# Kernel tuning notes

Hardware: AMD Instinct MI355X
Metric: run time of the kernel (lower is better)

Reference implementation:

```python
import jax, jax.numpy as jnp
import numpy as np
from jax import lax

B, C, H, W = 8, 64, 50, 65
K = 3
N = H * W            # 3250 attention positions
NR = N - 1           # 3249 = 57^2 rotary positions (first token unrotated)
SIDE = float(np.sqrt(NR))  # 57.0, exact
THETA = 10.0
EPS = 1e-5


def setup_inputs() -> dict:
    key = jax.random.key(0)
    ks = jax.random.split(key, 6)
    x = jax.random.normal(ks[0], (B, C, H, W), jnp.float32)
    s = 1.0 / np.sqrt(C * K * K)
    wq = jax.random.normal(ks[1], (C, C, K, K), jnp.float32) * s
    wk = jax.random.normal(ks[2], (C, C, K, K), jnp.float32) * s
    wv = jax.random.normal(ks[3], (C, C, K, K), jnp.float32) * s
    bq = jnp.zeros((C,), jnp.float32)
    bk = jnp.zeros((C,), jnp.float32)
    bv = jnp.zeros((C,), jnp.float32)
    # init_2d_freqs with num_heads=1, rotate=True, viewed as (2, C//2)
    mag = 1.0 / THETA ** (jnp.arange(0, C, 4, dtype=jnp.float32)[: C // 4] / C)
    ang = float(jax.random.uniform(ks[4])) * 2.0 * np.pi
    fx = jnp.concatenate([mag * np.cos(ang), mag * np.cos(np.pi / 2 + ang)])
    fy = jnp.concatenate([mag * np.sin(ang), mag * np.sin(np.pi / 2 + ang)])
    freqs = jnp.stack([fx, fy], axis=0)  # (2, C//2)
    gamma = jnp.zeros((1,), jnp.float32)
    bn_weight = jnp.ones((C,), jnp.float32)
    bn_bias = jnp.zeros((C,), jnp.float32)
    return {"x": x, "wq": wq, "bq": bq, "wk": wk, "bk": bk, "wv": wv,
            "bv": bv, "freqs": freqs, "gamma": gamma,
            "bn_weight": bn_weight, "bn_bias": bn_bias}


def _conv(x, w, b):
    y = lax.conv_general_dilated(x, w, (1, 1), 'SAME',
                                 dimension_numbers=('NCHW', 'OIHW', 'NCHW'))
    return y + b[None, :, None, None]


def _forward(x, wq, bq, wk, bk, wv, bv, freqs, gamma, bn_weight, bn_bias):
    q = _conv(x, wq, bq)
    k = _conv(x, wk, bk)
    v = _conv(x, wv, bv)

    # mixed RoPE angles on a sqrt(N-1) x sqrt(N-1) grid (compute_mixed_cis)
    t = jnp.arange(NR, dtype=jnp.float32)
    t_x = jnp.mod(t, SIDE)
    t_y = jnp.floor(t / SIDE)
    angles = t_x[:, None] * freqs[0][None, :] + t_y[:, None] * freqs[1][None, :]  # (NR, C//2)
    cos, sin = jnp.cos(angles), jnp.sin(angles)

    def rot(seq):  # (B, NR, C) -> rotate consecutive pairs by angles
        p = seq.reshape(B, NR, C // 2, 2)
        a, b = p[..., 0], p[..., 1]
        return jnp.stack([a * cos - b * sin, a * sin + b * cos], axis=-1).reshape(B, NR, C)

    qf = q.reshape(B, C, N).transpose(0, 2, 1)  # (B, N, C)
    kf = k.reshape(B, C, N).transpose(0, 2, 1)
    q_rot = jnp.concatenate([qf[:, :1], rot(qf[:, 1:])], axis=1)
    k_rot = jnp.concatenate([kf[:, :1], rot(kf[:, 1:])], axis=1)

    energy = jnp.einsum('bnc,bmc->bnm', q_rot, k_rot)  # (B, N, N)
    att = jax.nn.softmax(energy, axis=-1)
    vf = v.reshape(B, C, N)
    # out[b,c,m] = sum_n v[b,c,n] * att[b,m,n]
    out = jnp.einsum('bcn,bmn->bcm', vf, att).reshape(B, C, H, W)

    y = gamma * x + out
    # BatchNorm2d in training mode: batch statistics over (N, H, W)
    mean = jnp.mean(y, axis=(0, 2, 3), keepdims=True)
    var = jnp.var(y, axis=(0, 2, 3), keepdims=True)
    yn = (y - mean) * lax.rsqrt(var + EPS)
    return yn * bn_weight[None, :, None, None] + bn_bias[None, :, None, None]


def reference(x, wq, bq, wk, bk, wv, bv, freqs, gamma, bn_weight, bn_bias):
    return _forward(x, wq, bq, wk, bk, wv, bv, freqs, gamma, bn_weight, bn_bias)
```

## Files before the change

### kernel.cpp

```cpp
#include <hip/hip_runtime.h>
#include <math.h>

#define B_ 8
#define C_ 64
#define H_ 50
#define W_ 65
#define N_ 3250
#define NP_ 3264
#define SIDE_ 57.0f
#define EPS_ 1e-5f

typedef __attribute__((ext_vector_type(4))) float f32x4;
typedef __attribute__((ext_vector_type(8))) short s16x8;

__device__ __forceinline__ unsigned short rne_bf16(float f) {
    unsigned u = __builtin_bit_cast(unsigned, f);
    u += 0x7FFFu + ((u >> 16) & 1u);
    return (unsigned short)(u >> 16);
}
__device__ __forceinline__ float bf16_f(unsigned short h) {
    return __builtin_bit_cast(float, (unsigned)h << 16);
}

#define MFMA16(acc, a, b) \
    (acc) = __builtin_amdgcn_mfma_f32_16x16x32_bf16((a), (b), (acc), 0, 0, 0)

__global__ void k_wprep(const float* __restrict__ wq, const float* __restrict__ wk,
                        const float* __restrict__ wv,
                        unsigned short* __restrict__ wt_hi, unsigned short* __restrict__ wt_lo)
{
    const int idx  = blockIdx.x * 256 + threadIdx.x;
    const int slot = idx >> 11;
    const int rem  = idx & 2047;
    const int co   = rem >> 5;
    const int kk   = rem & 31;
    const int cvv  = slot / 18;
    const int r2   = slot % 18;
    const int khkw = r2 >> 1;
    const int chunk= r2 & 1;
    const float* wp = (cvv == 0) ? wq : ((cvv == 1) ? wk : wv);
    const float v = wp[co * 576 + (chunk * 32 + kk) * 9 + khkw];
    const unsigned short hh = rne_bf16(v);
    wt_hi[idx] = hh;
    wt_lo[idx] = rne_bf16(v - bf16_f(hh));
}

__global__ __launch_bounds__(256) void k_xprep(
    const float* __restrict__ x,
    unsigned short* __restrict__ xt_hi, unsigned short* __restrict__ xt_lo)
{
    const int row = blockIdx.x;
    const int b   = blockIdx.y;
    const int t   = threadIdx.x;
    __shared__ float xls[64 * 66];
    const size_t ob = (size_t)(b * 52 + row) * 68 * 64;
    if (row == 0 || row == 51) {
        for (int s = t; s < 68 * 64; s += 256) { xt_hi[ob + s] = 0; xt_lo[ob + s] = 0; }
        return;
    }
    const int h = row - 1;
    for (int s = t; s < 64 * 65; s += 256) {
        const int ci = s / 65, w = s % 65;
        xls[ci * 66 + w] = x[((size_t)(b * 64 + ci) * 50 + h) * 65 + w];
    }
    __syncthreads();
    for (int s = t; s < 68 * 64; s += 256) {
        const int ci = s & 63, wq = s >> 6;
        const float v = (wq >= 1 && wq <= 65) ? xls[ci * 66 + (wq - 1)] : 0.f;
        const unsigned short hh = rne_bf16(v);
        xt_hi[ob + s] = hh;
        xt_lo[ob + s] = rne_bf16(v - bf16_f(hh));
    }
}

__global__ void k_trig(const float* __restrict__ fr, float* __restrict__ tt)
{
    const int idx = blockIdx.x * 256 + threadIdx.x;
    if (idx >= 3249 * 32) return;
    const int p = idx & 31;
    const float fi = (float)(idx >> 5);
    const float ty = floorf(fi / SIDE_);
    const float tx = fi - ty * SIDE_;
    float sn, cs;
    sincosf(tx * fr[p] + ty * fr[32 + p], &sn, &cs);
    tt[idx * 2]     = cs;
    tt[idx * 2 + 1] = sn;
}

__global__ __launch_bounds__(256) void k_conv2(
    const unsigned short* __restrict__ xt_hi, const unsigned short* __restrict__ xt_lo,
    const unsigned short* __restrict__ wt_hi, const unsigned short* __restrict__ wt_lo,
    const float* __restrict__ bq, const float* __restrict__ bk, const float* __restrict__ bv,
    const float* __restrict__ tt,
    float* __restrict__ qr, unsigned short* __restrict__ khg,
    unsigned short* __restrict__ klg, unsigned short* __restrict__ vgT)
{
    const int h  = blockIdx.x;
    const int b  = blockIdx.y;
    const int cv = blockIdx.z;
    const int t  = threadIdx.x;
    const int l  = t & 63;
    const int nt = t >> 6;
    const int c  = l & 15;
    const int g  = l >> 4;

    __shared__ unsigned short vt[64 * 68];

    const float* bp = (cv == 0) ? bq : ((cv == 1) ? bk : bv);
    const int mstart[5] = {0, 16, 32, 48, 49};

    const f32x4 zero4 = {0.f, 0.f, 0.f, 0.f};
    f32x4 acc[5];
#pragma unroll
    for (int mt = 0; mt < 5; ++mt) acc[mt] = zero4;

#pragma unroll 1
    for (int chunk = 0; chunk < 2; ++chunk) {
#pragma unroll 1
        for (int khkw = 0; khkw < 9; ++khkw) {
            const int kh = khkw / 3, kw = khkw % 3;
            const int wb = ((cv * 18 + khkw * 2 + chunk) << 11) + (nt * 16 + c) * 32 + g * 8;
            const s16x8 bh = *(const s16x8*)(wt_hi + wb);
            const s16x8 bl = *(const s16x8*)(wt_lo + wb);
            const int ab0 = (((b * 52 + h + kh) * 68) + c + kw) * 64 + chunk * 32 + g * 8;
#pragma unroll
            for (int mt = 0; mt < 5; ++mt) {
                const int ai = ab0 + mstart[mt] * 64;
                const s16x8 ah = *(const s16x8*)(xt_hi + ai);
                const s16x8 al = *(const s16x8*)(xt_lo + ai);
                MFMA16(acc[mt], ah, bh);
                MFMA16(acc[mt], al, bh);
                MFMA16(acc[mt], ah, bl);
            }
        }
    }

    const int co = nt * 16 + c;
    const float bias = bp[co];

    if (cv == 2) {
#pragma unroll
        for (int mt = 0; mt < 5; ++mt)
#pragma unroll
            for (int r = 0; r < 4; ++r) {
                const int mloc = mstart[mt] + g * 4 + r;
                vt[co * 68 + mloc] = rne_bf16(acc[mt][r] + bias);
            }
        __syncthreads();
        for (int s = t; s < 64 * 65; s += 256) {
            const int cc = s / 65, mm = s % 65;
            vgT[(size_t)(b * 64 + cc) * NP_ + h * 65 + mm] = vt[cc * 68 + mm];
        }
        return;
    }

#pragma unroll
    for (int mt = 0; mt < 5; ++mt)
#pragma unroll
        for (int r = 0; r < 4; ++r) {
            const int mloc = mstart[mt] + g * 4 + r;
            const int pos  = h * 65 + mloc;
            float v = acc[mt][r] + bias;
            const float pr = __shfl_xor(v, 1);
            if (pos > 0) {
                const float2 cs2 = *(const float2*)(tt + ((size_t)(pos - 1) * 32 + (co >> 1)) * 2);
                v = (l & 1) ? (pr * cs2.y + v * cs2.x) : (v * cs2.x - pr * cs2.y);
            }
            if (cv == 0) {
                qr[(size_t)(b * N_ + pos) * 64 + co] = v;
            } else {
                const size_t idx = (size_t)(b * NP_ + pos) * 64 + co;
                const unsigned short hh = rne_bf16(v);
                khg[idx] = hh;
                klg[idx] = rne_bf16(v - bf16_f(hh));
            }
        }
}

__global__ __launch_bounds__(512) void k_flash5(
    const float* __restrict__ qr, const unsigned short* __restrict__ khg,
    const unsigned short* __restrict__ klg, const unsigned short* __restrict__ vgT,
    float* __restrict__ oo)
{
    const int b  = blockIdx.x;
    const int t  = threadIdx.x;
    const int wz = t >> 6;
    const int l  = t & 63;
    const int c  = l & 15;
    const int g  = l >> 4;
    const int m0 = blockIdx.y * 128 + wz * 16;

    __shared__ __align__(16) unsigned short kbh[4096];
    __shared__ __align__(16) unsigned short kbl[4096];
    __shared__ __align__(16) unsigned short vb[4096];
    __shared__ __align__(16) char psmem[32768];

    char* pwh = psmem + wz * 4096;
    char* pwl = psmem + wz * 4096 + 2048;

    s16x8 qh[2], ql[2];
#pragma unroll
    for (int ks = 0; ks < 2; ++ks) {
        const float* qp = qr + ((size_t)(b * N_ + m0 + c) * 64 + ks * 32 + g * 8);
        const f32x4 f0 = *(const f32x4*)qp;
        const f32x4 f1 = *(const f32x4*)(qp + 4);
#pragma unroll
        for (int j = 0; j < 4; ++j) {
            const unsigned short h0 = rne_bf16(f0[j]);
            qh[ks][j]     = (short)h0;
            ql[ks][j]     = (short)rne_bf16(f0[j] - bf16_f(h0));
            const unsigned short h1 = rne_bf16(f1[j]);
            qh[ks][4 + j] = (short)h1;
            ql[ks][4 + j] = (short)rne_bf16(f1[j] - bf16_f(h1));
        }
    }

    const f32x4 zero4 = {0.f, 0.f, 0.f, 0.f};
    f32x4 osum[4];
#pragma unroll
    for (int ct = 0; ct < 4; ++ct) osum[ct] = zero4;
    float run_m[4], run_l[4];
#pragma unroll
    for (int r = 0; r < 4; ++r) { run_m[r] = -1e30f; run_l[r] = 0.f; }

    const int srow   = t >> 3;
    const int schunk = t & 7;
    const int sdst   = (srow * 128 + schunk * 16) ^ ((srow & 7) << 4);

    for (int tile = 0; tile < 51; ++tile) {
        const int n0 = tile << 6;

        __syncthreads();
        {
            const unsigned short* ksrc = khg + ((size_t)(b * NP_) + n0) * 64;
            const unsigned short* lsrc = klg + ((size_t)(b * NP_) + n0) * 64;
            const unsigned short* vsrc = vgT + (size_t)(b * 64 + srow) * NP_ + n0;
            *(s16x8*)((char*)kbh + sdst) = *(const s16x8*)(ksrc + t * 8);
            *(s16x8*)((char*)kbl + sdst) = *(const s16x8*)(lsrc + t * 8);
            *(s16x8*)((char*)vb  + sdst) = *(const s16x8*)(vsrc + schunk * 8);
        }
        __syncthreads();

        f32x4 s4[4];
#pragma unroll
        for (int nt = 0; nt < 4; ++nt) s4[nt] = zero4;
#pragma unroll
        for (int ks = 0; ks < 2; ++ks) {
#pragma unroll
            for (int nt = 0; nt < 4; ++nt) {
                const int krow = nt * 16 + c;
                const int koff = (krow * 128 + ks * 64 + g * 16) ^ ((krow & 7) << 4);
                const s16x8 kh = *(const s16x8*)((const char*)kbh + koff);
                const s16x8 kl = *(const s16x8*)((const char*)kbl + koff);
                MFMA16(s4[nt], qh[ks], kh);
                MFMA16(s4[nt], ql[ks], kh);
                MFMA16(s4[nt], qh[ks], kl);
            }
        }

        if (tile == 50) {
#pragma unroll
            for (int nt = 0; nt < 4; ++nt)
                if (n0 + nt * 16 + c >= N_) {
                    const f32x4 m4 = {-1e30f, -1e30f, -1e30f, -1e30f};
                    s4[nt] = m4;
                }
        }

        float corr[4];
#pragma unroll
        for (int r = 0; r < 4; ++r) {
            float tm = fmaxf(fmaxf(s4[0][r], s4[1][r]), fmaxf(s4[2][r], s4[3][r]));
            tm = fmaxf(tm, __shfl_xor(tm, 1));
            tm = fmaxf(tm, __shfl_xor(tm, 2));
            tm = fmaxf(tm, __shfl_xor(tm, 4));
            tm = fmaxf(tm, __shfl_xor(tm, 8));
            const float mnew = fmaxf(run_m[r], tm);
            corr[r] = __expf(run_m[r] - mnew);
            float ts = 0.f;
#pragma unroll
            for (int nt = 0; nt < 4; ++nt) {
                const float p = __expf(s4[nt][r] - mnew);
                s4[nt][r] = p;
                ts += p;
            }
            ts += __shfl_xor(ts, 1);
            ts += __shfl_xor(ts, 2);
            ts += __shfl_xor(ts, 4);
            ts += __shfl_xor(ts, 8);
            run_l[r] = run_l[r] * corr[r] + ts;
            run_m[r] = mnew;
        }
#pragma unroll
        for (int ct = 0; ct < 4; ++ct)
#pragma unroll
            for (int r = 0; r < 4; ++r) osum[ct][r] *= corr[r];

#pragma unroll
        for (int nt = 0; nt < 4; ++nt)
#pragma unroll
            for (int r = 0; r < 4; ++r) {
                const int m   = g * 4 + r;
                const int off = m * 128 + ((((nt * 16 + c) * 2)) ^ ((m & 7) << 4));
                const float p = s4[nt][r];
                const unsigned short ph = rne_bf16(p);
                *(unsigned short*)(pwh + off) = ph;
                *(unsigned short*)(pwl + off) = rne_bf16(p - bf16_f(ph));
            }

#pragma unroll
        for (int ks = 0; ks < 2; ++ks) {
            const int aoff = c * 128 + (((ks * 64 + g * 16)) ^ ((c & 7) << 4));
            const s16x8 pah = *(const s16x8*)(pwh + aoff);
            const s16x8 pal = *(const s16x8*)(pwl + aoff);
#pragma unroll
            for (int ct = 0; ct < 4; ++ct) {
                const int vrow = ct * 16 + c;
                const int voff = (vrow * 128 + ks * 64 + g * 16) ^ ((vrow & 7) << 4);
                const s16x8 vf = *(const s16x8*)((const char*)vb + voff);
                MFMA16(osum[ct], pah, vf);
                MFMA16(osum[ct], pal, vf);
            }
        }
    }

#pragma unroll
    for (int ct = 0; ct < 4; ++ct)
#pragma unroll
        for (int r = 0; r < 4; ++r) {
            const int m = m0 + g * 4 + r;
            if (m < N_) oo[(size_t)(b * N_ + m) * 64 + ct * 16 + c] = osum[ct][r] / run_l[r];
        }
}

__global__ __launch_bounds__(256) void k_bnstats(
    const float* __restrict__ x, const float* __restrict__ oo,
    const float* __restrict__ gamma, float* __restrict__ yy, float* __restrict__ part)
{
    const int b    = blockIdx.y;
    const int m0   = blockIdx.x * 64;
    const int t    = threadIdx.x;
    const int lane = t & 63;
    const int blk  = blockIdx.y * 51 + blockIdx.x;
    __shared__ float ot[64 * 65];
    const float gm = gamma[0];
    {
        const int r4 = t >> 6;
#pragma unroll
        for (int i = 0; i < 16; ++i) {
            const int row = r4 + i * 4;
            const int m   = m0 + row;
            ot[row * 65 + lane] = (m < N_) ? oo[((size_t)b * N_ + m) * 64 + lane] : 0.f;
        }
    }
    __syncthreads();
    const int  m     = m0 + lane;
    const bool valid = (m < N_);
#pragma unroll
    for (int i = 0; i < 16; ++i) {
        const int c = (t >> 6) + (i << 2);
        float y = 0.f;
        if (valid) {
            const float xv = x[(size_t)(b * 64 + c) * N_ + m];
            y = gm * xv + ot[lane * 65 + c];
            yy[(size_t)(b * 64 + c) * N_ + m] = y;
        }
        float s1 = y, s2 = y * y;
#pragma unroll
        for (int d = 1; d < 64; d <<= 1) { s1 += __shfl_xor(s1, d); s2 += __shfl_xor(s2, d); }
        if (lane == 0) {
            part[(size_t)blk * 128 + c]      = s1;
            part[(size_t)blk * 128 + 64 + c] = s2;
        }
    }
}

__global__ void k_bnfin(const float* __restrict__ part, const float* __restrict__ bnw,
                        const float* __restrict__ bnb, float* __restrict__ ss)
{
    const int c = threadIdx.x;
    float s1 = 0.f, s2 = 0.f;
    for (int k = 0; k < 408; ++k) {
        s1 += part[(size_t)k * 128 + c];
        s2 += part[(size_t)k * 128 + 64 + c];
    }
    const float cnt  = (float)(B_ * N_);
    const float mean = s1 / cnt;
    const float var  = s2 / cnt - mean * mean;
    const float sc   = bnw[c] * rsqrtf(var + EPS_);
    ss[c]      = sc;
    ss[64 + c] = bnb[c] - mean * sc;
}

__global__ __launch_bounds__(256) void k_bnapply(
    const float* __restrict__ yy, const float* __restrict__ ss, float* __restrict__ out)
{
    const int total = B_ * C_ * N_;
    for (int e = blockIdx.x * 256 + threadIdx.x; e < total; e += gridDim.x * 256) {
        const int c = (e / N_) & 63;
        out[e] = yy[e] * ss[c] + ss[64 + c];
    }
}

extern "C" void kernel_launch(void* const* d_in, const int* in_sizes, int n_in,
                              void* d_out, int out_size, void* d_ws, size_t ws_size,
                              hipStream_t stream) {
    const float* x     = (const float*)d_in[0];
    const float* wq    = (const float*)d_in[1];
    const float* bq    = (const float*)d_in[2];
    const float* wk    = (const float*)d_in[3];
    const float* bk    = (const float*)d_in[4];
    const float* wv    = (const float*)d_in[5];
    const float* bv    = (const float*)d_in[6];
    const float* fr    = (const float*)d_in[7];
    const float* gamma = (const float*)d_in[8];
    const float* bnw   = (const float*)d_in[9];
    const float* bnb   = (const float*)d_in[10];

    float* wsf = (float*)d_ws;
    float*          qr    = wsf;
    unsigned short* khg   = (unsigned short*)(wsf + 1664000);
    unsigned short* klg   = (unsigned short*)(wsf + 2499584);
    unsigned short* vgT   = (unsigned short*)(wsf + 3335168);
    float*          regB  = wsf + 4170752;
    unsigned short* xt_hi = (unsigned short*)regB;
    unsigned short* xt_lo = (unsigned short*)(regB + 905216);
    unsigned short* wt_hi = (unsigned short*)(regB + 1810432);
    unsigned short* wt_lo = (unsigned short*)(regB + 1865728);
    float*          tt    = regB + 1921024;
    float*          oo    = regB;
    float*          part  = wsf + 6299712;
    float*          ss    = wsf + 6351936;
    float*          yy    = qr;
    float*          outp  = (float*)d_out;

    k_wprep<<<432, 256, 0, stream>>>(wq, wk, wv, wt_hi, wt_lo);
    k_xprep<<<dim3(52, 8), 256, 0, stream>>>(x, xt_hi, xt_lo);
    k_trig<<<407, 256, 0, stream>>>(fr, tt);
    k_conv2<<<dim3(50, 8, 3), 256, 0, stream>>>(xt_hi, xt_lo, wt_hi, wt_lo,
                                                bq, bk, bv, tt, qr, khg, klg, vgT);
    k_flash5<<<dim3(8, 26), 512, 0, stream>>>(qr, khg, klg, vgT, oo);
    k_bnstats<<<dim3(51, 8), 256, 0, stream>>>(x, oo, gamma, yy, part);
    k_bnfin<<<1, 64, 0, stream>>>(part, bnw, bnb, ss);
    k_bnapply<<<1024, 256, 0, stream>>>(yy, ss, outp);
}
```

Before: 389.0 us.

## Double-buffer K/V tiles in flash kernel with register prefetch

```diff
diff --git a/kernel.cpp b/kernel.cpp
--- a/kernel.cpp
+++ b/kernel.cpp
@@ -177,7 +177,7 @@
         }
 }
 
-__global__ __launch_bounds__(512) void k_flash5(
+__global__ __launch_bounds__(512) void k_flash6(
     const float* __restrict__ qr, const unsigned short* __restrict__ khg,
     const unsigned short* __restrict__ klg, const unsigned short* __restrict__ vgT,
     float* __restrict__ oo)
@@ -190,9 +190,9 @@
     const int g  = l >> 4;
     const int m0 = blockIdx.y * 128 + wz * 16;
 
-    __shared__ __align__(16) unsigned short kbh[4096];
-    __shared__ __align__(16) unsigned short kbl[4096];
-    __shared__ __align__(16) unsigned short vb[4096];
+    __shared__ __align__(16) unsigned short kbh[2][4096];
+    __shared__ __align__(16) unsigned short kbl[2][4096];
+    __shared__ __align__(16) unsigned short vb [2][4096];
     __shared__ __align__(16) char psmem[32768];
 
     char* pwh = psmem + wz * 4096;
@@ -226,20 +226,29 @@
     const int srow   = t >> 3;
     const int schunk = t & 7;
     const int sdst   = (srow * 128 + schunk * 16) ^ ((srow & 7) << 4);
+    const unsigned short* kbase = khg + (size_t)(b * NP_) * 64;
+    const unsigned short* lbase = klg + (size_t)(b * NP_) * 64;
+    const unsigned short* vbase = vgT + (size_t)(b * 64 + srow) * NP_;
+
+    s16x8 rk = *(const s16x8*)(kbase + t * 8);
+    s16x8 rl = *(const s16x8*)(lbase + t * 8);
+    s16x8 rv = *(const s16x8*)(vbase + schunk * 8);
 
     for (int tile = 0; tile < 51; ++tile) {
-        const int n0 = tile << 6;
-
+        const int n0  = tile << 6;
+        const int cur = tile & 1;
+
+        *(s16x8*)((char*)kbh[cur] + sdst) = rk;
+        *(s16x8*)((char*)kbl[cur] + sdst) = rl;
+        *(s16x8*)((char*)vb [cur] + sdst) = rv;
         __syncthreads();
-        {
-            const unsigned short* ksrc = khg + ((size_t)(b * NP_) + n0) * 64;
-            const unsigned short* lsrc = klg + ((size_t)(b * NP_) + n0) * 64;
-            const unsigned short* vsrc = vgT + (size_t)(b * 64 + srow) * NP_ + n0;
-            *(s16x8*)((char*)kbh + sdst) = *(const s16x8*)(ksrc + t * 8);
-            *(s16x8*)((char*)kbl + sdst) = *(const s16x8*)(lsrc + t * 8);
-            *(s16x8*)((char*)vb  + sdst) = *(const s16x8*)(vsrc + schunk * 8);
-        }
-        __syncthreads();
+
+        if (tile < 50) {
+            const int n1 = (tile + 1) << 6;
+            rk = *(const s16x8*)(kbase + (size_t)n1 * 64 + t * 8);
+            rl = *(const s16x8*)(lbase + (size_t)n1 * 64 + t * 8);
+            rv = *(const s16x8*)(vbase + n1 + schunk * 8);
+        }
 
         f32x4 s4[4];
 #pragma unroll
@@ -250,8 +259,8 @@
             for (int nt = 0; nt < 4; ++nt) {
                 const int krow = nt * 16 + c;
                 const int koff = (krow * 128 + ks * 64 + g * 16) ^ ((krow & 7) << 4);
-                const s16x8 kh = *(const s16x8*)((const char*)kbh + koff);
-                const s16x8 kl = *(const s16x8*)((const char*)kbl + koff);
+                const s16x8 kh = *(const s16x8*)((const char*)kbh[cur] + koff);
+                const s16x8 kl = *(const s16x8*)((const char*)kbl[cur] + koff);
                 MFMA16(s4[nt], qh[ks], kh);
                 MFMA16(s4[nt], ql[ks], kh);
                 MFMA16(s4[nt], qh[ks], kl);
@@ -317,7 +326,7 @@
             for (int ct = 0; ct < 4; ++ct) {
                 const int vrow = ct * 16 + c;
                 const int voff = (vrow * 128 + ks * 64 + g * 16) ^ ((vrow & 7) << 4);
-                const s16x8 vf = *(const s16x8*)((const char*)vb + voff);
+                const s16x8 vf = *(const s16x8*)((const char*)vb[cur] + voff);
                 MFMA16(osum[ct], pah, vf);
                 MFMA16(osum[ct], pal, vf);
             }
@@ -439,7 +448,7 @@
     k_trig<<<407, 256, 0, stream>>>(fr, tt);
     k_conv2<<<dim3(50, 8, 3), 256, 0, stream>>>(xt_hi, xt_lo, wt_hi, wt_lo,
                                                 bq, bk, bv, tt, qr, khg, klg, vgT);
-    k_flash5<<<dim3(8, 26), 512, 0, stream>>>(qr, khg, klg, vgT, oo);
+    k_flash6<<<dim3(8, 26), 512, 0, stream>>>(qr, khg, klg, vgT, oo);
     k_bnstats<<<dim3(51, 8), 256, 0, stream>>>(x, oo, gamma, yy, part);
     k_bnfin<<<1, 64, 0, stream>>>(part, bnw, bnb, ss);
     k_bnapply<<<1024, 256, 0, stream>>>(yy, ss, outp);
```

Measured after the change: 369.9 us. -4.9%, faster.
